# Kernel tuning notes

Measured on AMD Instinct MI355X. Metric: run time of the kernel, lower is better.

## Reference

```python
import jax, jax.numpy as jnp
import numpy as np

TWO_PI = 2.0 * np.pi
DAMP_VERTICAL = 1.0
DAMP_HORIZONTAL = 0.0


def _var(p, q, ra, rb, wvno, xka, xkb, dpth):
    # surf96 'var': layer eigenfunction products with evanescent-scaling (exp(-pex-sex))
    ra_s = jnp.where(ra > 0, ra, 1.0)
    rb_s = jnp.where(rb > 0, rb, 1.0)
    # P branch
    sinp_o = jnp.sin(p)
    fac_p = jnp.where(p < 16.0, jnp.exp(-2.0 * p), 0.0)
    cosp_e = (1.0 + fac_p) * 0.5
    sinp_e = (1.0 - fac_p) * 0.5
    lt_a = wvno < xka
    gt_a = wvno > xka
    pex = jnp.where(gt_a, p, 0.0)
    cosp = jnp.where(lt_a, jnp.cos(p), jnp.where(gt_a, cosp_e, 1.0))
    w = jnp.where(lt_a, sinp_o / ra_s, jnp.where(gt_a, sinp_e / ra_s, dpth))
    x = jnp.where(lt_a, -ra * sinp_o, jnp.where(gt_a, ra * sinp_e, 0.0))
    # S branch
    sinq_o = jnp.sin(q)
    fac_q = jnp.where(q < 16.0, jnp.exp(-2.0 * q), 0.0)
    cosq_e = (1.0 + fac_q) * 0.5
    sinq_e = (1.0 - fac_q) * 0.5
    lt_b = wvno < xkb
    gt_b = wvno > xkb
    sex = jnp.where(gt_b, q, 0.0)
    cosq = jnp.where(lt_b, jnp.cos(q), jnp.where(gt_b, cosq_e, 1.0))
    y = jnp.where(lt_b, sinq_o / rb_s, jnp.where(gt_b, sinq_e / rb_s, dpth))
    z = jnp.where(lt_b, -rb * sinq_o, jnp.where(gt_b, rb * sinq_e, 0.0))
    exa = pex + sex
    a0 = jnp.where(exa < 60.0, jnp.exp(-exa), 0.0)
    return (a0, cosp * cosq, cosp * y, cosp * z, cosq * w, cosq * x,
            x * y, x * z, w * y, w * z)


def _dnka(wvno2, gam, gammk, rho, a0, cpcq, cpy, cpz, cqw, cqx, xy, xz, wy, wz):
    # Dunkin's 5x5 compound matrix
    gamm1 = gam - 1.0
    twgm1 = gam + gamm1
    gmgmk = gam * gammk
    gmgm1 = gam * gamm1
    gm1sq = gamm1 * gamm1
    rho2 = rho * rho
    a0pq = a0 - cpcq
    t = -2.0 * wvno2
    c00 = cpcq - 2.0 * gmgm1 * a0pq - gmgmk * xz - wvno2 * gm1sq * wy
    c01 = (wvno2 * cpy - cqx) / rho
    c02 = -(twgm1 * a0pq + gammk * xz + wvno2 * gamm1 * wy) / rho
    c03 = (cpz - wvno2 * cqw) / rho
    c04 = -(2.0 * wvno2 * a0pq + xz + wvno2 * wvno2 * wy) / rho2
    c10 = (gmgmk * cpz - gm1sq * cqw) * rho
    c11 = cpcq
    c12 = gammk * cpz - gamm1 * cqw
    c13 = -wz
    c30 = (gm1sq * cpy - gmgmk * cqx) * rho
    c31 = -xy
    c32 = gamm1 * cpy - gammk * cqx
    c40 = -(2.0 * gmgmk * gm1sq * a0pq + gmgmk * gmgmk * xz + gm1sq * gm1sq * wy) * rho2
    c42 = -(gammk * gamm1 * twgm1 * a0pq + gam * gammk * gammk * xz + gamm1 * gm1sq * wy) * rho
    c20 = t * c42
    c21 = t * c32
    c22 = a0 + 2.0 * (cpcq - c00)
    c23 = t * c12
    c24 = t * c02
    rows = [[c00, c01, c02, c03, c04],
            [c10, c11, c12, c13, c03],
            [c20, c21, c22, c23, c24],
            [c30, c31, c32, c11, c01],
            [c40, c30, c42, c10, c00]]
    return jnp.stack([jnp.stack(r, axis=-1) for r in rows], axis=-2)


def _dltar4(wvno, omega, d, a, b, rho):
    # Rayleigh secular function, Dunkin algorithm, no water layer (llw=-1).
    # wvno/omega: (M, *extra) broadcast-compatible; d,a,b,rho: (M, L)
    extra = wvno.ndim - 1
    L = d.shape[-1]

    def lay(x):  # (M, L) -> (L, M, 1, ..., 1)
        return jnp.moveaxis(x, -1, 0).reshape((L, x.shape[0]) + (1,) * extra)

    dL, aL, bL, rhoL = lay(d), lay(a), lay(b), lay(rho)
    omega = jnp.maximum(omega, 1.0e-4)
    wvno2 = wvno * wvno

    # bottom half-space E vector
    xka = omega / aL[L - 1]
    xkb = omega / bL[L - 1]
    ra = jnp.sqrt(jnp.abs(wvno2 - xka * xka))
    rb = jnp.sqrt(jnp.abs(wvno2 - xkb * xkb))
    t = bL[L - 1] / omega
    gammk = 2.0 * t * t
    gam = gammk * wvno2
    gamm1 = gam - 1.0
    r = rhoL[L - 1]
    e = jnp.stack([r * r * (gamm1 * gamm1 - gam * gammk * ra * rb),
                   -r * ra,
                   r * (gamm1 - gammk * ra * rb),
                   r * rb,
                   wvno2 - ra * rb], axis=-1)

    xs = (dL[L - 2::-1], aL[L - 2::-1], bL[L - 2::-1], rhoL[L - 2::-1])

    def step(e, layer):
        dm, am, bm, rm = layer
        xka = omega / am
        xkb = omega / bm
        t = bm / omega
        gammk = 2.0 * t * t
        gam = gammk * wvno2
        ra = jnp.sqrt(jnp.abs(wvno2 - xka * xka))
        rb = jnp.sqrt(jnp.abs(wvno2 - xkb * xkb))
        p = ra * dm
        q = rb * dm
        vt = _var(p, q, ra, rb, wvno, xka, xkb, dm)
        ca = _dnka(wvno2, gam, gammk, rm, *vt)  # (..., 5, 5)
        ee = jnp.einsum('...j,...ji->...i', e, ca)
        t1 = jnp.max(jnp.abs(ee), axis=-1, keepdims=True)
        t1 = jnp.where(t1 < 1.0e-30, 1.0, t1)  # normc numerical-stability rescale
        return ee / t1, None

    e, _ = jax.lax.scan(step, e, xs)
    return e[..., 0]


def _forward(vlist, tlist, d, b, Clist):
    # Brocher empirical relations (initial_method == 'Brocher')
    a = 0.9409 + 2.0947 * b - 0.8206 * b**2 + 0.2683 * b**3 - 0.0251 * b**4
    rho = 1.6612 * a - 0.4721 * a**2 + 0.0671 * a**3 - 0.0043 * a**4 + 0.000106 * a**5

    omega = TWO_PI / tlist          # (M, P)
    wvno = omega / vlist
    e00 = _dltar4(wvno, omega, d, a, b, rho)  # (M, P)

    # normalization grid (torch.no_grad -> stop_gradient)
    omega_g = omega[:, None, :]                   # (M, 1, P)
    wvno_g = omega_g / Clist[None, :, None]       # (M, NC, P)
    det = jax.lax.stop_gradient(_dltar4(wvno_g, omega_g, d, a, b, rho))  # (M, NC, P)

    rng = jnp.max(det, axis=1) - jnp.min(det, axis=1)  # (M, P)
    e00 = e00 / rng
    e00 = jnp.power(0.1, jnp.abs(e00)) - 1.0           # compress_method == 'exp'
    e00_all = jnp.sum(jnp.abs(e00), axis=1) / e00.shape[-1]  # (M,)

    # vertical / horizontal damping regularization
    M, Lv = b.shape
    ev = jnp.eye(Lv, dtype=b.dtype)
    Lmat_v = 2.0 * ev - jnp.eye(Lv, k=1, dtype=b.dtype) - jnp.eye(Lv, k=-1, dtype=b.dtype)
    Lmat_v = Lmat_v.at[0, 0].set(1.0).at[Lv - 1, Lv - 1].set(1.0)
    eh = jnp.eye(M, dtype=b.dtype)
    Lmat_h = 2.0 * eh - jnp.eye(M, k=1, dtype=b.dtype) - jnp.eye(M, k=-1, dtype=b.dtype)
    Lmat_h = Lmat_h.at[0, 0].set(1.0).at[M - 1, M - 1].set(1.0)
    m_v = DAMP_VERTICAL * jnp.einsum('ij,mj->mi', Lmat_v, b) / Lv
    m_h = DAMP_HORIZONTAL * jnp.einsum('nm,ml->nl', Lmat_h, b) / Lv
    return e00_all + jnp.sum(jnp.abs(m_v), axis=1) + jnp.sum(jnp.abs(m_h), axis=1)


def setup_inputs() -> dict:
    key = jax.random.key(0)
    k1, k2, k3, k4 = jax.random.split(key, 4)
    M, L, P, NC = 64, 32, 100, 400
    tlist = jnp.sort(0.5 + 9.5 * jax.random.uniform(k1, (M, P), dtype=jnp.float32), axis=1)  # periods (s)
    vlist = 1.2 + 2.8 * jax.random.uniform(k2, (M, P), dtype=jnp.float32)                    # phase vel (km/s)
    d = 0.2 + 0.8 * jax.random.uniform(k3, (M, L), dtype=jnp.float32)                        # thickness (km)
    b = jnp.sort(1.5 + 3.0 * jax.random.uniform(k4, (M, L), dtype=jnp.float32), axis=1)      # Vs (km/s)
    Clist = jnp.linspace(1.0, 4.8, NC, dtype=jnp.float32)
    return {"vlist": vlist, "tlist": tlist, "d": d, "b": b, "Clist": Clist}


def reference(vlist, tlist, d, b, Clist):
    return _forward(vlist, tlist, d, b, Clist)
```

## Files before the change

### kernel.cpp

```cpp
#include <hip/hip_runtime.h>
#include <math.h>
#include <float.h>

#define Mdim 64
#define Ldim 32
#define Pdim 100
#define NCdim 400
#define EVALS_PER_P (NCdim + 1)
#define EVALS_PER_WAVE 128
#define WAVES_PER_M 314
#define BLOCKS_PER_M 79
#define NPTS (Mdim * Pdim)
#define TWO_PI_F 6.28318530717958647692f
#define INV_2PI_F 0.15915494309189535f
#define NLOG2E_F (-1.4426950408889634f)
#define LOG2_10TH (-3.3219280948873623f)

typedef float v2 __attribute__((ext_vector_type(2)));

__device__ __forceinline__ v2 mk2(float a, float b) { v2 r; r.x = a; r.y = b; return r; }
__device__ __forceinline__ v2 sel2(bool cx, bool cy, v2 a, v2 b) {
    return mk2(cx ? a.x : b.x, cy ? a.y : b.y);
}

struct alignas(16) LayerP {
    float dm;
    float inv_a2;
    float inv_b2;
    float b2two;
    float rm;
    float inv_rm;
    float inv_rho2;
    float rho2;
};

__device__ __forceinline__ unsigned ord_encode(float f) {
    unsigned u = __float_as_uint(f);
    return (u & 0x80000000u) ? ~u : (u | 0x80000000u);
}
__device__ __forceinline__ float ord_decode(unsigned u) {
    unsigned v = (u & 0x80000000u) ? (u & 0x7FFFFFFFu) : ~u;
    return __uint_as_float(v);
}

template <bool RENORM>
__device__ __forceinline__ void layer_step(const LayerP& L,
                                           v2 wvno2, v2 wvno4, v2 tneg, v2 om2, v2 invom2,
                                           v2& e0, v2& e1, v2& e2, v2& e3, v2& e4)
{
    const float dm = L.dm;

    const v2 ra2 = wvno2 - om2 * L.inv_a2;
    const v2 rb2 = wvno2 - om2 * L.inv_b2;

    const v2 inv_ra = mk2(__builtin_amdgcn_rsqf(fabsf(ra2.x)),
                          __builtin_amdgcn_rsqf(fabsf(ra2.y)));
    const v2 inv_rb = mk2(__builtin_amdgcn_rsqf(fabsf(rb2.x)),
                          __builtin_amdgcn_rsqf(fabsf(rb2.y)));
    const v2 ra = mk2(fabsf(ra2.x), fabsf(ra2.y)) * inv_ra;
    const v2 rb = mk2(fabsf(rb2.x), fabsf(rb2.y)) * inv_rb;
    const v2 pp = ra * dm;
    const v2 qq = rb * dm;
    const v2 gammk = L.b2two * invom2;
    const v2 gam   = gammk * wvno2;

    const v2 ppr = pp * INV_2PI_F;
    const v2 qqr = qq * INV_2PI_F;
    const v2 sp = mk2(__builtin_amdgcn_sinf(ppr.x), __builtin_amdgcn_sinf(ppr.y));
    const v2 cp = mk2(__builtin_amdgcn_cosf(ppr.x), __builtin_amdgcn_cosf(ppr.y));
    const v2 sq = mk2(__builtin_amdgcn_sinf(qqr.x), __builtin_amdgcn_sinf(qqr.y));
    const v2 cq = mk2(__builtin_amdgcn_cosf(qqr.x), __builtin_amdgcn_cosf(qqr.y));
    const v2 pe = pp * NLOG2E_F;
    const v2 qe = qq * NLOG2E_F;
    const v2 e_p = mk2(__builtin_amdgcn_exp2f(pe.x), __builtin_amdgcn_exp2f(pe.y));
    const v2 e_q = mk2(__builtin_amdgcn_exp2f(qe.x), __builtin_amdgcn_exp2f(qe.y));

    const v2 fac_p = e_p * e_p;
    const v2 fac_q = e_q * e_q;
    const v2 cosp_e = 0.5f * fac_p + 0.5f;
    const v2 sinp_e = -0.5f * fac_p + 0.5f;
    const v2 cosq_e = 0.5f * fac_q + 0.5f;
    const v2 sinq_e = -0.5f * fac_q + 0.5f;

    const bool lt_ax = ra2.x < 0.0f, lt_ay = ra2.y < 0.0f;
    const bool lt_bx = rb2.x < 0.0f, lt_by = rb2.y < 0.0f;

    const v2 one = mk2(1.0f, 1.0f);
    const v2 cosp = sel2(lt_ax, lt_ay, cp, cosp_e);
    const v2 w = sel2(lt_ax, lt_ay, sp, sinp_e) * inv_ra;
    const v2 cosq = sel2(lt_bx, lt_by, cq, cosq_e);
    const v2 y = sel2(lt_bx, lt_by, sq, sinq_e) * inv_rb;
    const v2 a0 = sel2(lt_ax, lt_ay, one, e_p) * sel2(lt_bx, lt_by, one, e_q);

    const v2 cpcq = cosp * cosq;
    const v2 cpy  = cosp * y;
    const v2 cqw  = cosq * w;
    const v2 wy   = w * y;
    const v2 cpz  = rb2 * cpy;
    const v2 cqx  = ra2 * cqw;
    const v2 wz   = rb2 * wy;
    const v2 xy   = ra2 * wy;
    const v2 xz   = ra2 * wz;

    const v2 gamm1 = gam - 1.0f;
    const v2 twgm1 = gam + gamm1;
    const v2 gmgmk = gam * gammk;
    const v2 gmgm1 = gam * gamm1;
    const v2 gm1sq = gamm1 * gamm1;
    const v2 a0pq  = a0 - cpcq;

    const v2 c00 = cpcq - 2.0f * gmgm1 * a0pq - gmgmk * xz - wvno2 * gm1sq * wy;
    const v2 c01 = (wvno2 * cpy - cqx) * L.inv_rm;
    const v2 c02 = -(twgm1 * a0pq + gammk * xz + wvno2 * gamm1 * wy) * L.inv_rm;
    const v2 c03 = (cpz - wvno2 * cqw) * L.inv_rm;
    const v2 c04 = -(2.0f * wvno2 * a0pq + xz + wvno4 * wy) * L.inv_rho2;
    const v2 c10 = (gmgmk * cpz - gm1sq * cqw) * L.rm;
    const v2 c11 = cpcq;
    const v2 c12 = gammk * cpz - gamm1 * cqw;
    const v2 c13 = -wz;
    const v2 c30 = (gm1sq * cpy - gmgmk * cqx) * L.rm;
    const v2 c31 = -xy;
    const v2 c32 = gamm1 * cpy - gammk * cqx;
    const v2 c40 = -(2.0f * gmgmk * gm1sq * a0pq + gmgmk * gmgmk * xz
                     + gm1sq * gm1sq * wy) * L.rho2;
    const v2 c42 = -(gammk * gamm1 * twgm1 * a0pq + gam * gammk * gammk * xz
                     + gamm1 * gm1sq * wy) * L.rm;
    const v2 c22 = a0 + 2.0f * (cpcq - c00);

    const v2 et2 = tneg * e2;

    const v2 ee0 = e0 * c00 + e1 * c10 + et2 * c42 + e3 * c30 + e4 * c40;
    const v2 ee1 = e0 * c01 + e1 * c11 + et2 * c32 + e3 * c31 + e4 * c30;
    const v2 ee2 = e0 * c02 + e1 * c12 + e2  * c22 + e3 * c32 + e4 * c42;
    const v2 ee3 = e0 * c03 + e1 * c13 + et2 * c12 + e3 * c11 + e4 * c10;
    const v2 ee4 = e0 * c04 + e1 * c03 + et2 * c02 + e3 * c01 + e4 * c00;

    if constexpr (RENORM) {
        float t1x = fmaxf(fmaxf(fabsf(ee0.x), fabsf(ee1.x)), fabsf(ee2.x));
        t1x = fmaxf(t1x, fmaxf(fabsf(ee3.x), fabsf(ee4.x)));
        float t1y = fmaxf(fmaxf(fabsf(ee0.y), fabsf(ee1.y)), fabsf(ee2.y));
        t1y = fmaxf(t1y, fmaxf(fabsf(ee3.y), fabsf(ee4.y)));
        t1x = fmaxf(t1x, 1e-30f);
        t1y = fmaxf(t1y, 1e-30f);
        const v2 inv = mk2(__builtin_amdgcn_rcpf(t1x), __builtin_amdgcn_rcpf(t1y));
        e0 = ee0 * inv;
        e1 = ee1 * inv;
        e2 = ee2 * inv;
        e3 = ee3 * inv;
        e4 = ee4 * inv;
    } else {
        e0 = ee0; e1 = ee1; e2 = ee2; e3 = ee3; e4 = ee4;
    }
}

__device__ __forceinline__ v2 dltar4_pk(v2 wvno2, v2 om2, v2 invom2,
                                        const LayerP* __restrict__ slay)
{
    const v2 wvno4 = wvno2 * wvno2;
    const v2 tneg  = -2.0f * wvno2;

    const LayerP H = slay[Ldim - 1];
    const v2 ra2h = wvno2 - om2 * H.inv_a2;
    const v2 rb2h = wvno2 - om2 * H.inv_b2;
    const v2 ra_h = mk2(__builtin_amdgcn_sqrtf(fabsf(ra2h.x)),
                        __builtin_amdgcn_sqrtf(fabsf(ra2h.y)));
    const v2 rb_h = mk2(__builtin_amdgcn_sqrtf(fabsf(rb2h.x)),
                        __builtin_amdgcn_sqrtf(fabsf(rb2h.y)));
    const v2 gammk_h = H.b2two * invom2;
    const v2 gam_h   = gammk_h * wvno2;
    const v2 gamm1_h = gam_h - 1.0f;
    const v2 rarb_h  = ra_h * rb_h;
    v2 e0 = H.rho2 * (gamm1_h * gamm1_h - gam_h * gammk_h * rarb_h);
    v2 e1 = -H.rm * ra_h;
    v2 e2 = H.rm * (gamm1_h - gammk_h * rarb_h);
    v2 e3 = H.rm * rb_h;
    v2 e4 = wvno2 - rarb_h;

    layer_step<true>(slay[Ldim - 2], wvno2, wvno4, tneg, om2, invom2,
                     e0, e1, e2, e3, e4);
    for (int l = Ldim - 3; l >= 1; l -= 2) {
        layer_step<false>(slay[l],     wvno2, wvno4, tneg, om2, invom2,
                          e0, e1, e2, e3, e4);
        layer_step<true> (slay[l - 1], wvno2, wvno4, tneg, om2, invom2,
                          e0, e1, e2, e3, e4);
    }
    return e0;
}

__global__ void init_ws_kernel(unsigned* __restrict__ mxU, unsigned* __restrict__ mnU)
{
    int i = blockIdx.x * blockDim.x + threadIdx.x;
    if (i < NPTS) {
        mxU[i] = 0u;
        mnU[i] = 0xFFFFFFFFu;
    }
}

__global__ __launch_bounds__(256, 5)
void disp_kernel(const float* __restrict__ vlist, const float* __restrict__ tlist,
                 const float* __restrict__ dth,  const float* __restrict__ bvel,
                 const float* __restrict__ Clist,
                 unsigned* __restrict__ mxU, unsigned* __restrict__ mnU,
                 float* __restrict__ e00f)
{
    __shared__ LayerP slay[Ldim];

    const int bid = blockIdx.x;
    const int m   = bid / BLOCKS_PER_M;
    const int wb  = bid - m * BLOCKS_PER_M;
    const int tid  = threadIdx.x;
    const int wid  = tid >> 6;
    const int lane = tid & 63;
    const int wv   = wb * 4 + wid;

    if (tid < Ldim) {
        const float bb = bvel[m * Ldim + tid];
        const float b2 = bb * bb;
        const float b3 = b2 * bb;
        const float b4 = b2 * b2;
        const float aa = 0.9409f + 2.0947f * bb - 0.8206f * b2
                         + 0.2683f * b3 - 0.0251f * b4;
        const float a2 = aa * aa;
        const float a3 = a2 * aa;
        const float a4 = a2 * a2;
        const float a5 = a4 * aa;
        const float rr = 1.6612f * aa - 0.4721f * a2 + 0.0671f * a3
                         - 0.0043f * a4 + 0.000106f * a5;
        LayerP Lp;
        Lp.dm       = dth[m * Ldim + tid];
        Lp.inv_a2   = 1.0f / (aa * aa);
        Lp.inv_b2   = 1.0f / (bb * bb);
        Lp.b2two    = 2.0f * bb * bb;
        Lp.rm       = rr;
        Lp.inv_rm   = 1.0f / rr;
        Lp.inv_rho2 = 1.0f / (rr * rr);
        Lp.rho2     = rr * rr;
        slay[tid] = Lp;
    }
    __syncthreads();

    if (wv >= WAVES_PER_M) return;

    const int S  = wv * EVALS_PER_WAVE;
    const int p0 = S / EVALS_PER_P;
    const int c0 = S - p0 * EVALS_PER_P;

    int cx = c0 + lane;
    const bool crx = cx >= EVALS_PER_P;
    const int px = p0 + (crx ? 1 : 0);
    cx = crx ? cx - EVALS_PER_P : cx;
    const bool validx = px < Pdim;

    int cy = c0 + 64 + lane;
    const bool cry = cy >= EVALS_PER_P;
    const int py = p0 + (cry ? 1 : 0);
    cy = cry ? cy - EVALS_PER_P : cy;
    const bool validy = py < Pdim;

    const int mpx = m * Pdim + (validx ? px : 0);
    const int mpy = m * Pdim + (validy ? py : 0);
    const float omx = fmaxf(TWO_PI_F / tlist[mpx], 1.0e-4f);
    const float omy = fmaxf(TWO_PI_F / tlist[mpy], 1.0e-4f);
    const bool isCx = cx < NCdim;
    const bool isCy = cy < NCdim;
    const float denx = isCx ? Clist[cx] : vlist[mpx];
    const float deny = isCy ? Clist[cy] : vlist[mpy];
    const float wvx = omx / denx;
    const float wvy = omy / deny;

    const v2 om2    = mk2(omx * omx, omy * omy);
    const v2 invom2 = mk2(__builtin_amdgcn_rcpf(om2.x), __builtin_amdgcn_rcpf(om2.y));
    const v2 wvno2  = mk2(wvx * wvx, wvy * wvy);

    const v2 det = dltar4_pk(wvno2, om2, invom2, slay);

    if (validx && !isCx) e00f[m * Pdim + px] = det.x;
    if (validy && !isCy) e00f[m * Pdim + py] = det.y;

    const int pA = p0;
    const int pB = p0 + ((c0 + EVALS_PER_WAVE - 1) >= EVALS_PER_P ? 1 : 0);

    {
        const bool inAx = validx && isCx && (px == pA);
        const bool inAy = validy && isCy && (py == pA);
        float mxA = fmaxf(inAx ? det.x : -FLT_MAX, inAy ? det.y : -FLT_MAX);
        float mnA = fminf(inAx ? det.x :  FLT_MAX, inAy ? det.y :  FLT_MAX);
        for (int off = 32; off >= 1; off >>= 1) {
            mxA = fmaxf(mxA, __shfl_xor(mxA, off));
            mnA = fminf(mnA, __shfl_xor(mnA, off));
        }
        if (lane == 0 && pA < Pdim) {
            atomicMax(&mxU[m * Pdim + pA], ord_encode(mxA));
            atomicMin(&mnU[m * Pdim + pA], ord_encode(mnA));
        }
    }
    if (pB != pA) {
        const bool inBx = validx && isCx && (px == pB);
        const bool inBy = validy && isCy && (py == pB);
        float mxB = fmaxf(inBx ? det.x : -FLT_MAX, inBy ? det.y : -FLT_MAX);
        float mnB = fminf(inBx ? det.x :  FLT_MAX, inBy ? det.y :  FLT_MAX);
        for (int off = 32; off >= 1; off >>= 1) {
            mxB = fmaxf(mxB, __shfl_xor(mxB, off));
            mnB = fminf(mnB, __shfl_xor(mnB, off));
        }
        if (lane == 0 && pB < Pdim) {
            atomicMax(&mxU[m * Pdim + pB], ord_encode(mxB));
            atomicMin(&mnU[m * Pdim + pB], ord_encode(mnB));
        }
    }
}

__global__ __launch_bounds__(64)
void epilogue_kernel(const unsigned* __restrict__ mxU, const unsigned* __restrict__ mnU,
                     const float* __restrict__ e00f, const float* __restrict__ bvel,
                     float* __restrict__ out)
{
    const int m    = blockIdx.x;
    const int lane = threadIdx.x;

    float acc = 0.0f;
    for (int p = lane; p < Pdim; p += 64) {
        const int i = m * Pdim + p;
        const float mx = ord_decode(mxU[i]);
        const float mn = ord_decode(mnU[i]);
        const float en = e00f[i] / (mx - mn);
        acc += 1.0f - __builtin_amdgcn_exp2f(fabsf(en) * LOG2_10TH);
    }

    float damp = 0.0f;
    if (lane < Ldim) {
        const float bb    = bvel[m * Ldim + lane];
        const float bprev = bvel[m * Ldim + ((lane == 0) ? 0 : lane - 1)];
        const float bnext = bvel[m * Ldim + ((lane == Ldim - 1) ? Ldim - 1 : lane + 1)];
        float tval;
        if (lane == 0)             tval = bb - bnext;
        else if (lane == Ldim - 1) tval = bb - bprev;
        else                       tval = 2.0f * bb - bprev - bnext;
        damp = fabsf(tval * (1.0f / (float)Ldim));
    }

    float tot = fmaf(acc, 1.0f / (float)Pdim, damp);
    for (int off = 32; off >= 1; off >>= 1)
        tot += __shfl_xor(tot, off);
    if (lane == 0) out[m] = tot;
}

extern "C" void kernel_launch(void* const* d_in, const int* in_sizes, int n_in,
                              void* d_out, int out_size, void* d_ws, size_t ws_size,
                              hipStream_t stream)
{
    const float* vlist = (const float*)d_in[0];
    const float* tlist = (const float*)d_in[1];
    const float* dth   = (const float*)d_in[2];
    const float* bvel  = (const float*)d_in[3];
    const float* Clist = (const float*)d_in[4];
    float* out = (float*)d_out;

    unsigned* mxU = (unsigned*)d_ws;
    unsigned* mnU = mxU + NPTS;
    float*    e00f = (float*)(mnU + NPTS);

    hipLaunchKernelGGL(init_ws_kernel, dim3((NPTS + 255) / 256), dim3(256), 0, stream,
                       mxU, mnU);
    hipLaunchKernelGGL(disp_kernel, dim3(Mdim * BLOCKS_PER_M), dim3(256), 0, stream,
                       vlist, tlist, dth, bvel, Clist, mxU, mnU, e00f);
    hipLaunchKernelGGL(epilogue_kernel, dim3(Mdim), dim3(64), 0, stream,
                       mxU, mnU, e00f, bvel, out);
}
```

Baseline: 252.7 us.

## Replace atomic min/max with per-wave partial slots and drop init kernel

Each wave now writes its per-period max/min partials to a dedicated slot instead of doing ordered-integer atomicMax/atomicMin. The epilogue reduces those slots per period, which removes the workspace init kernel launch and atomic contention. The wavenumber division is also replaced by a hardware reciprocal multiply, which is slightly less accurate. The epilogue does more loads per period but is small.

```diff
diff --git a/kernel.cpp b/kernel.cpp
--- a/kernel.cpp
+++ b/kernel.cpp
@@ -11,6 +11,7 @@
 #define WAVES_PER_M 314
 #define BLOCKS_PER_M 79
 #define NPTS (Mdim * Pdim)
+#define WSLOT (Mdim * WAVES_PER_M)
 #define TWO_PI_F 6.28318530717958647692f
 #define INV_2PI_F 0.15915494309189535f
 #define NLOG2E_F (-1.4426950408889634f)
@@ -33,15 +34,6 @@
     float inv_rho2;
     float rho2;
 };
-
-__device__ __forceinline__ unsigned ord_encode(float f) {
-    unsigned u = __float_as_uint(f);
-    return (u & 0x80000000u) ? ~u : (u | 0x80000000u);
-}
-__device__ __forceinline__ float ord_decode(unsigned u) {
-    unsigned v = (u & 0x80000000u) ? (u & 0x7FFFFFFFu) : ~u;
-    return __uint_as_float(v);
-}
 
 template <bool RENORM>
 __device__ __forceinline__ void layer_step(const LayerP& L,
@@ -187,20 +179,12 @@
     return e0;
 }
 
-__global__ void init_ws_kernel(unsigned* __restrict__ mxU, unsigned* __restrict__ mnU)
-{
-    int i = blockIdx.x * blockDim.x + threadIdx.x;
-    if (i < NPTS) {
-        mxU[i] = 0u;
-        mnU[i] = 0xFFFFFFFFu;
-    }
-}
-
 __global__ __launch_bounds__(256, 5)
 void disp_kernel(const float* __restrict__ vlist, const float* __restrict__ tlist,
                  const float* __restrict__ dth,  const float* __restrict__ bvel,
                  const float* __restrict__ Clist,
-                 unsigned* __restrict__ mxU, unsigned* __restrict__ mnU,
+                 float* __restrict__ pAmx, float* __restrict__ pAmn,
+                 float* __restrict__ pBmx, float* __restrict__ pBmn,
                  float* __restrict__ e00f)
 {
     __shared__ LayerP slay[Ldim];
@@ -265,8 +249,8 @@
     const bool isCy = cy < NCdim;
     const float denx = isCx ? Clist[cx] : vlist[mpx];
     const float deny = isCy ? Clist[cy] : vlist[mpy];
-    const float wvx = omx / denx;
-    const float wvy = omy / deny;
+    const float wvx = omx * __builtin_amdgcn_rcpf(denx);
+    const float wvy = omy * __builtin_amdgcn_rcpf(deny);
 
     const v2 om2    = mk2(omx * omx, omy * omy);
     const v2 invom2 = mk2(__builtin_amdgcn_rcpf(om2.x), __builtin_amdgcn_rcpf(om2.y));
@@ -279,6 +263,7 @@
 
     const int pA = p0;
     const int pB = p0 + ((c0 + EVALS_PER_WAVE - 1) >= EVALS_PER_P ? 1 : 0);
+    const int slot = m * WAVES_PER_M + wv;
 
     {
         const bool inAx = validx && isCx && (px == pA);
@@ -289,9 +274,9 @@
             mxA = fmaxf(mxA, __shfl_xor(mxA, off));
             mnA = fminf(mnA, __shfl_xor(mnA, off));
         }
-        if (lane == 0 && pA < Pdim) {
-            atomicMax(&mxU[m * Pdim + pA], ord_encode(mxA));
-            atomicMin(&mnU[m * Pdim + pA], ord_encode(mnA));
+        if (lane == 0) {
+            pAmx[slot] = mxA;
+            pAmn[slot] = mnA;
         }
     }
     if (pB != pA) {
@@ -304,14 +289,15 @@
             mnB = fminf(mnB, __shfl_xor(mnB, off));
         }
         if (lane == 0 && pB < Pdim) {
-            atomicMax(&mxU[m * Pdim + pB], ord_encode(mxB));
-            atomicMin(&mnU[m * Pdim + pB], ord_encode(mnB));
+            pBmx[slot] = mxB;
+            pBmn[slot] = mnB;
         }
     }
 }
 
 __global__ __launch_bounds__(64)
-void epilogue_kernel(const unsigned* __restrict__ mxU, const unsigned* __restrict__ mnU,
+void epilogue_kernel(const float* __restrict__ pAmx, const float* __restrict__ pAmn,
+                     const float* __restrict__ pBmx, const float* __restrict__ pBmn,
                      const float* __restrict__ e00f, const float* __restrict__ bvel,
                      float* __restrict__ out)
 {
@@ -320,10 +306,18 @@
 
     float acc = 0.0f;
     for (int p = lane; p < Pdim; p += 64) {
-        const int i = m * Pdim + p;
-        const float mx = ord_decode(mxU[i]);
-        const float mn = ord_decode(mnU[i]);
-        const float en = e00f[i] / (mx - mn);
+        const int w0 = (EVALS_PER_P * p) / EVALS_PER_WAVE;
+        const int w1 = (EVALS_PER_P * p + NCdim - 1) / EVALS_PER_WAVE;
+        float mx = -FLT_MAX, mn = FLT_MAX;
+        for (int w = w0; w <= w1; ++w) {
+            const int s = m * WAVES_PER_M + w;
+            const int pAw = (w * EVALS_PER_WAVE) / EVALS_PER_P;
+            const float vmx = (pAw == p) ? pAmx[s] : pBmx[s];
+            const float vmn = (pAw == p) ? pAmn[s] : pBmn[s];
+            mx = fmaxf(mx, vmx);
+            mn = fminf(mn, vmn);
+        }
+        const float en = e00f[m * Pdim + p] / (mx - mn);
         acc += 1.0f - __builtin_amdgcn_exp2f(fabsf(en) * LOG2_10TH);
     }
 
@@ -356,14 +350,14 @@
     const float* Clist = (const float*)d_in[4];
     float* out = (float*)d_out;
 
-    unsigned* mxU = (unsigned*)d_ws;
-    unsigned* mnU = mxU + NPTS;
-    float*    e00f = (float*)(mnU + NPTS);
-
-    hipLaunchKernelGGL(init_ws_kernel, dim3((NPTS + 255) / 256), dim3(256), 0, stream,
-                       mxU, mnU);
+    float* pAmx = (float*)d_ws;
+    float* pAmn = pAmx + WSLOT;
+    float* pBmx = pAmn + WSLOT;
+    float* pBmn = pBmx + WSLOT;
+    float* e00f = pBmn + WSLOT;
+
     hipLaunchKernelGGL(disp_kernel, dim3(Mdim * BLOCKS_PER_M), dim3(256), 0, stream,
-                       vlist, tlist, dth, bvel, Clist, mxU, mnU, e00f);
+                       vlist, tlist, dth, bvel, Clist, pAmx, pAmn, pBmx, pBmn, e00f);
     hipLaunchKernelGGL(epilogue_kernel, dim3(Mdim), dim3(64), 0, stream,
-                       mxU, mnU, e00f, bvel, out);
-}
+                       pAmx, pAmn, pBmx, pBmn, e00f, bvel, out);
+}
```

Measured after the change: 252.3 us (median of 2 runs). No clear change (-0.2%).
